# Optimization experiments

Measured on AMD Instinct MI355X. Metric: run time of the kernel, lower is better.

The kernel has to match this reference:

```python
import jax, jax.numpy as jnp
import numpy as np

IN_SIZE = 65536
HIDDEN = 128
D_STEPS = 64   # nd_actions[0]
N_ACT = 512    # nd_actions[1]


def setup_inputs() -> dict:
    key = jax.random.key(0)
    ks = jax.random.split(key, 7)
    s = 1.0 / np.sqrt(HIDDEN)  # torch LSTMCell/Linear init scale (uniform); use scaled normal
    return {
        "x": jax.random.normal(ks[0], (IN_SIZE,), jnp.float32),
        "w_ih": jax.random.normal(ks[1], (4 * HIDDEN, IN_SIZE), jnp.float32) * s,
        "w_hh": jax.random.normal(ks[2], (4 * HIDDEN, HIDDEN), jnp.float32) * s,
        "b_ih": jax.random.normal(ks[3], (4 * HIDDEN,), jnp.float32) * s,
        "b_hh": jax.random.normal(ks[4], (4 * HIDDEN,), jnp.float32) * s,
        "w_lin": jax.random.normal(ks[5], (N_ACT, HIDDEN), jnp.float32) * s,
        "b_lin": jax.random.normal(ks[6], (N_ACT,), jnp.float32) * s,
    }


def reference(x, w_ih, w_hh, b_ih, b_hh, w_lin, b_lin):
    # x is constant across the D steps, so its gate contribution is computed once.
    ihx = w_ih @ x + b_ih + b_hh  # (4H,)
    h0 = jnp.zeros((HIDDEN,), x.dtype)
    c0 = jnp.zeros((HIDDEN,), x.dtype)

    def step(carry, _):
        h, c = carry
        gates = ihx + w_hh @ h  # (4H,)
        i, f, g, o = jnp.split(gates, 4)  # torch LSTMCell gate order: i, f, g, o
        c = jax.nn.sigmoid(f) * c + jax.nn.sigmoid(i) * jnp.tanh(g)
        h = jax.nn.sigmoid(o) * jnp.tanh(c)
        logits = w_lin @ h + b_lin  # (N,)
        return (h, c), logits

    _, action_probs = jax.lax.scan(step, (h0, c0), None, length=D_STEPS)
    return action_probs  # (D, N)
```

## Files before the change

kernel.cpp:

```cpp
#include <hip/hip_runtime.h>
#include <hip/hip_bf16.h>

#define IN_SIZE 65536
#define HIDDEN 128
#define D_STEPS 64
#define N_ACT 512

typedef _Float16 half2_ __attribute__((ext_vector_type(2)));

__device__ __forceinline__ float dot2f(half2_ a, half2_ b, float c) {
#if __has_builtin(__builtin_amdgcn_fdot2)
    return __builtin_amdgcn_fdot2(a, b, c, false);
#else
    return c + (float)a[0] * (float)b[0] + (float)a[1] * (float)b[1];
#endif
}

__global__ __launch_bounds__(256) void k_ihx(const float* __restrict__ w_ih,
                                             const float* __restrict__ x,
                                             float* __restrict__ partials) {
    int bid = blockIdx.x;
    int r = bid >> 2;
    int c = bid & 3;
    int t = threadIdx.x;
    const float4* wp = (const float4*)(w_ih + (size_t)r * IN_SIZE + c * 16384);
    const float4* xp = (const float4*)(x + c * 16384);
    float acc = 0.f;
#pragma unroll
    for (int i = 0; i < 16; ++i) {
        float4 w4 = wp[t + i * 256];
        float4 x4 = xp[t + i * 256];
        acc += w4.x * x4.x + w4.y * x4.y + w4.z * x4.z + w4.w * x4.w;
    }
#pragma unroll
    for (int off = 32; off; off >>= 1) acc += __shfl_down(acc, off, 64);
    __shared__ float s[4];
    if ((t & 63) == 0) s[t >> 6] = acc;
    __syncthreads();
    if (t == 0) partials[r * 4 + c] = s[0] + s[1] + s[2] + s[3];
}

__global__ __launch_bounds__(512) void k_rec(const float* __restrict__ w_hh,
                                             const float* __restrict__ b_ih,
                                             const float* __restrict__ b_hh,
                                             const float* __restrict__ partials,
                                             float* __restrict__ h_hist) {
    int t = threadIdx.x;
    int l = t & 63;
    int gate = t & 3;
    int cell = t >> 2;
    int row = gate * HIDDEN + cell;

    half2_ wr[HIDDEN / 2];
    const float2* wp = (const float2*)(w_hh + (size_t)row * HIDDEN);
#pragma unroll
    for (int i = 0; i < HIDDEN / 2; ++i) {
        float2 v = wp[i];
        half2_ w2 = {(_Float16)v.x, (_Float16)v.y};
        wr[i] = w2;
    }
    float ihx = partials[row * 4 + 0] + partials[row * 4 + 1] +
                partials[row * 4 + 2] + partials[row * 4 + 3] +
                b_ih[row] + b_hh[row];

    __shared__ half2_ h_s[2][HIDDEN / 2];
    float c = 0.f;
    if (t < HIDDEN / 2) { half2_ z = {(_Float16)0.f, (_Float16)0.f}; h_s[0][t] = z; }
    __syncthreads();

    for (int d = 0; d < D_STEPS; ++d) {
        int rb = d & 1, wb = rb ^ 1;
        const half2_* hb = h_s[rb];
        float a0 = 0.f, a1 = 0.f, a2 = 0.f, a3 = 0.f;
#pragma unroll
        for (int i = 0; i < HIDDEN / 2; i += 4) {
            a0 = dot2f(wr[i + 0], hb[i + 0], a0);
            a1 = dot2f(wr[i + 1], hb[i + 1], a1);
            a2 = dot2f(wr[i + 2], hb[i + 2], a2);
            a3 = dot2f(wr[i + 3], hb[i + 3], a3);
        }
        float g = ihx + ((a0 + a1) + (a2 + a3));
        float kmul = (gate == 2) ? 2.f : 1.f;
        float s = 1.f / (1.f + __expf(-kmul * g));
        float act = (gate == 2) ? (2.f * s - 1.f) : s;
        int base = l & ~3;
        float ai = __shfl(act, base + 0, 64);
        float af = __shfl(act, base + 1, 64);
        float at = __shfl(act, base + 2, 64);
        float ao = __shfl(act, base + 3, 64);
        c = af * c + ai * at;
        float h = ao * (2.f / (1.f + __expf(-2.f * c)) - 1.f);
        float hp = __shfl(h, (l + 4) & 63, 64);
        if ((t & 7) == 0) { half2_ p = {(_Float16)h, (_Float16)hp}; h_s[wb][t >> 3] = p; }
        if ((t & 3) == 0) h_hist[d * HIDDEN + cell] = h;
        __syncthreads();
    }
}

__global__ __launch_bounds__(512) void k_logits(const float* __restrict__ w_lin,
                                                const float* __restrict__ b_lin,
                                                const float* __restrict__ h_hist,
                                                float* __restrict__ out) {
    int d = blockIdx.x;
    int n = threadIdx.x;
    __shared__ float h_s[HIDDEN];
    if (n < HIDDEN) h_s[n] = h_hist[d * HIDDEN + n];
    __syncthreads();
    const float4* wp = (const float4*)(w_lin + (size_t)n * HIDDEN);
    float acc = b_lin[n];
#pragma unroll
    for (int k4 = 0; k4 < HIDDEN / 4; ++k4) {
        float4 w4 = wp[k4];
        acc += w4.x * h_s[4 * k4 + 0] + w4.y * h_s[4 * k4 + 1] +
               w4.z * h_s[4 * k4 + 2] + w4.w * h_s[4 * k4 + 3];
    }
    out[d * N_ACT + n] = acc;
}

extern "C" void kernel_launch(void* const* d_in, const int* in_sizes, int n_in,
                              void* d_out, int out_size, void* d_ws, size_t ws_size,
                              hipStream_t stream) {
    const float* x     = (const float*)d_in[0];
    const float* w_ih  = (const float*)d_in[1];
    const float* w_hh  = (const float*)d_in[2];
    const float* b_ih  = (const float*)d_in[3];
    const float* b_hh  = (const float*)d_in[4];
    const float* w_lin = (const float*)d_in[5];
    const float* b_lin = (const float*)d_in[6];
    float* out = (float*)d_out;

    float* ws       = (float*)d_ws;
    float* partials = ws;
    float* h_hist   = ws + 2048;

    k_ihx<<<2048, 256, 0, stream>>>(w_ih, x, partials);
    k_rec<<<1, 512, 0, stream>>>(w_hh, b_ih, b_hh, partials, h_hist);
    k_logits<<<64, 512, 0, stream>>>(w_lin, b_lin, h_hist, out);
}
```

Before: 83.67 us.

## Fuse three kernels into one persistent kernel with global atomic barriers

Replaces the three launches (ihx GEMV, serial recurrence, logits) with one persistent 256-block kernel that uses atomic-counter grid barriers between phases. Block 0 preloads w_hh while the ihx phase runs, and the h vector moves to half8 shared storage for wider loads. The aim is to remove launch gaps and the partials round-trip. In exchange it needs a memset per call, relies on all 256 blocks being co-resident for the spin barrier, and runs the w_ih stream with fewer, larger blocks.

```diff
diff --git a/kernel.cpp b/kernel.cpp
--- a/kernel.cpp
+++ b/kernel.cpp
@@ -5,8 +5,10 @@
 #define HIDDEN 128
 #define D_STEPS 64
 #define N_ACT 512
+#define NBLK 256
 
 typedef _Float16 half2_ __attribute__((ext_vector_type(2)));
+typedef _Float16 half8_ __attribute__((ext_vector_type(8)));
 
 __device__ __forceinline__ float dot2f(half2_ a, half2_ b, float c) {
 #if __has_builtin(__builtin_amdgcn_fdot2)
@@ -16,105 +18,131 @@
 #endif
 }
 
-__global__ __launch_bounds__(256) void k_ihx(const float* __restrict__ w_ih,
-                                             const float* __restrict__ x,
-                                             float* __restrict__ partials) {
-    int bid = blockIdx.x;
-    int r = bid >> 2;
-    int c = bid & 3;
-    int t = threadIdx.x;
-    const float4* wp = (const float4*)(w_ih + (size_t)r * IN_SIZE + c * 16384);
-    const float4* xp = (const float4*)(x + c * 16384);
-    float acc = 0.f;
-#pragma unroll
-    for (int i = 0; i < 16; ++i) {
-        float4 w4 = wp[t + i * 256];
-        float4 x4 = xp[t + i * 256];
-        acc += w4.x * x4.x + w4.y * x4.y + w4.z * x4.z + w4.w * x4.w;
+__device__ __forceinline__ void gbar(int* cnt) {
+    __syncthreads();
+    if (threadIdx.x == 0) {
+        __hip_atomic_fetch_add(cnt, 1, __ATOMIC_RELEASE, __HIP_MEMORY_SCOPE_AGENT);
+        while (__hip_atomic_load(cnt, __ATOMIC_ACQUIRE, __HIP_MEMORY_SCOPE_AGENT) < NBLK)
+            __builtin_amdgcn_s_sleep(8);
     }
-#pragma unroll
-    for (int off = 32; off; off >>= 1) acc += __shfl_down(acc, off, 64);
-    __shared__ float s[4];
-    if ((t & 63) == 0) s[t >> 6] = acc;
     __syncthreads();
-    if (t == 0) partials[r * 4 + c] = s[0] + s[1] + s[2] + s[3];
 }
 
-__global__ __launch_bounds__(512) void k_rec(const float* __restrict__ w_hh,
-                                             const float* __restrict__ b_ih,
-                                             const float* __restrict__ b_hh,
-                                             const float* __restrict__ partials,
-                                             float* __restrict__ h_hist) {
+__global__ __launch_bounds__(1024, 4) void fused(
+    const float* __restrict__ x,
+    const float* __restrict__ w_ih,
+    const float* __restrict__ w_hh,
+    const float* __restrict__ b_ih,
+    const float* __restrict__ b_hh,
+    const float* __restrict__ w_lin,
+    const float* __restrict__ b_lin,
+    int* __restrict__ cnt,
+    float* __restrict__ ihx_ws,
+    float* __restrict__ h_hist,
+    float* __restrict__ out) {
     int t = threadIdx.x;
-    int l = t & 63;
-    int gate = t & 3;
-    int cell = t >> 2;
-    int row = gate * HIDDEN + cell;
+    int b = blockIdx.x;
 
     half2_ wr[HIDDEN / 2];
-    const float2* wp = (const float2*)(w_hh + (size_t)row * HIDDEN);
+    int gate = t & 3;
+    int cell = (t >> 2) & 127;
+    if (b == 0 && t < 512) {
+        const float2* wp2 = (const float2*)(w_hh + (size_t)(gate * HIDDEN + cell) * HIDDEN);
 #pragma unroll
-    for (int i = 0; i < HIDDEN / 2; ++i) {
-        float2 v = wp[i];
-        half2_ w2 = {(_Float16)v.x, (_Float16)v.y};
-        wr[i] = w2;
+        for (int i = 0; i < HIDDEN / 2; ++i) {
+            float2 v = wp2[i];
+            half2_ w2 = {(_Float16)v.x, (_Float16)v.y};
+            wr[i] = w2;
+        }
     }
-    float ihx = partials[row * 4 + 0] + partials[row * 4 + 1] +
-                partials[row * 4 + 2] + partials[row * 4 + 3] +
-                b_ih[row] + b_hh[row];
 
-    __shared__ half2_ h_s[2][HIDDEN / 2];
-    float c = 0.f;
-    if (t < HIDDEN / 2) { half2_ z = {(_Float16)0.f, (_Float16)0.f}; h_s[0][t] = z; }
-    __syncthreads();
+    {
+        int q = t >> 9;
+        int u = t & 511;
+        int row = 2 * b + q;
+        const float4* wp = (const float4*)(w_ih + (size_t)row * IN_SIZE);
+        const float4* xp = (const float4*)x;
+        float acc = 0.f;
+#pragma unroll 8
+        for (int i = 0; i < 32; ++i) {
+            float4 w4 = wp[u + i * 512];
+            float4 x4 = xp[u + i * 512];
+            acc += w4.x * x4.x + w4.y * x4.y + w4.z * x4.z + w4.w * x4.w;
+        }
+#pragma unroll
+        for (int off = 32; off; off >>= 1) acc += __shfl_down(acc, off, 64);
+        __shared__ float s[16];
+        if ((t & 63) == 0) s[t >> 6] = acc;
+        __syncthreads();
+        if ((t & 511) == 0) {
+            float v = 0.f;
+#pragma unroll
+            for (int i = 0; i < 8; ++i) v += s[(q << 3) + i];
+            ihx_ws[row] = v + b_ih[row] + b_hh[row];
+        }
+    }
+    gbar(&cnt[0]);
 
-    for (int d = 0; d < D_STEPS; ++d) {
-        int rb = d & 1, wb = rb ^ 1;
-        const half2_* hb = h_s[rb];
-        float a0 = 0.f, a1 = 0.f, a2 = 0.f, a3 = 0.f;
+    __shared__ half8_ h_v[2][HIDDEN / 8];
+    if (b == 0) {
+        int l = t & 63;
+        float ihx = 0.f, c = 0.f;
+        if (t < 512) ihx = ihx_ws[gate * HIDDEN + cell];
+        if (t < HIDDEN) ((_Float16*)&h_v[0][0])[t] = (_Float16)0.f;
+        __syncthreads();
+
+        for (int d = 0; d < D_STEPS; ++d) {
+            int rbuf = d & 1, wbuf = rbuf ^ 1;
+            if (t < 512) {
+                const half8_* hb = h_v[rbuf];
+                float a0 = 0.f, a1 = 0.f, a2 = 0.f, a3 = 0.f;
 #pragma unroll
-        for (int i = 0; i < HIDDEN / 2; i += 4) {
-            a0 = dot2f(wr[i + 0], hb[i + 0], a0);
-            a1 = dot2f(wr[i + 1], hb[i + 1], a1);
-            a2 = dot2f(wr[i + 2], hb[i + 2], a2);
-            a3 = dot2f(wr[i + 3], hb[i + 3], a3);
+                for (int i = 0; i < 16; ++i) {
+                    union { half8_ v8; half2_ p[4]; } u;
+                    u.v8 = hb[i];
+                    a0 = dot2f(wr[4 * i + 0], u.p[0], a0);
+                    a1 = dot2f(wr[4 * i + 1], u.p[1], a1);
+                    a2 = dot2f(wr[4 * i + 2], u.p[2], a2);
+                    a3 = dot2f(wr[4 * i + 3], u.p[3], a3);
+                }
+                float g = ihx + ((a0 + a1) + (a2 + a3));
+                float kmul = (gate == 2) ? 2.f : 1.f;
+                float sg = 1.f / (1.f + __expf(-kmul * g));
+                float act = (gate == 2) ? (2.f * sg - 1.f) : sg;
+                int base = l & ~3;
+                float ai = __shfl(act, base + 0, 64);
+                float af = __shfl(act, base + 1, 64);
+                float at = __shfl(act, base + 2, 64);
+                float ao = __shfl(act, base + 3, 64);
+                c = af * c + ai * at;
+                float h = ao * (2.f / (1.f + __expf(-2.f * c)) - 1.f);
+                if ((t & 3) == 0) {
+                    ((_Float16*)&h_v[wbuf][0])[cell] = (_Float16)h;
+                    h_hist[d * HIDDEN + cell] = h;
+                }
+            }
+            __syncthreads();
         }
-        float g = ihx + ((a0 + a1) + (a2 + a3));
-        float kmul = (gate == 2) ? 2.f : 1.f;
-        float s = 1.f / (1.f + __expf(-kmul * g));
-        float act = (gate == 2) ? (2.f * s - 1.f) : s;
-        int base = l & ~3;
-        float ai = __shfl(act, base + 0, 64);
-        float af = __shfl(act, base + 1, 64);
-        float at = __shfl(act, base + 2, 64);
-        float ao = __shfl(act, base + 3, 64);
-        c = af * c + ai * at;
-        float h = ao * (2.f / (1.f + __expf(-2.f * c)) - 1.f);
-        float hp = __shfl(h, (l + 4) & 63, 64);
-        if ((t & 7) == 0) { half2_ p = {(_Float16)h, (_Float16)hp}; h_s[wb][t >> 3] = p; }
-        if ((t & 3) == 0) h_hist[d * HIDDEN + cell] = h;
+    }
+    gbar(&cnt[16]);
+
+    if (b < 32) {
+        int s3 = t >> 9;
+        int d = 2 * b + s3;
+        int n = t & 511;
+        __shared__ float hs2[2][HIDDEN];
+        if ((t & 511) < HIDDEN) hs2[s3][t & 127] = h_hist[d * HIDDEN + (t & 127)];
         __syncthreads();
+        const float4* wp = (const float4*)(w_lin + (size_t)n * HIDDEN);
+        float acc = b_lin[n];
+#pragma unroll
+        for (int k = 0; k < HIDDEN / 4; ++k) {
+            float4 w4 = wp[k];
+            acc += w4.x * hs2[s3][4 * k + 0] + w4.y * hs2[s3][4 * k + 1] +
+                   w4.z * hs2[s3][4 * k + 2] + w4.w * hs2[s3][4 * k + 3];
+        }
+        out[d * N_ACT + n] = acc;
     }
-}
-
-__global__ __launch_bounds__(512) void k_logits(const float* __restrict__ w_lin,
-                                                const float* __restrict__ b_lin,
-                                                const float* __restrict__ h_hist,
-                                                float* __restrict__ out) {
-    int d = blockIdx.x;
-    int n = threadIdx.x;
-    __shared__ float h_s[HIDDEN];
-    if (n < HIDDEN) h_s[n] = h_hist[d * HIDDEN + n];
-    __syncthreads();
-    const float4* wp = (const float4*)(w_lin + (size_t)n * HIDDEN);
-    float acc = b_lin[n];
-#pragma unroll
-    for (int k4 = 0; k4 < HIDDEN / 4; ++k4) {
-        float4 w4 = wp[k4];
-        acc += w4.x * h_s[4 * k4 + 0] + w4.y * h_s[4 * k4 + 1] +
-               w4.z * h_s[4 * k4 + 2] + w4.w * h_s[4 * k4 + 3];
-    }
-    out[d * N_ACT + n] = acc;
 }
 
 extern "C" void kernel_launch(void* const* d_in, const int* in_sizes, int n_in,
@@ -129,11 +157,12 @@
     const float* b_lin = (const float*)d_in[6];
     float* out = (float*)d_out;
 
-    float* ws       = (float*)d_ws;
-    float* partials = ws;
-    float* h_hist   = ws + 2048;
+    hipMemsetAsync(d_ws, 0, 128, stream);
+    int*   cnt    = (int*)d_ws;
+    float* ws_f   = (float*)d_ws;
+    float* ihx_ws = ws_f + 32;
+    float* h_hist = ws_f + 32 + 512;
 
-    k_ihx<<<2048, 256, 0, stream>>>(w_ih, x, partials);
-    k_rec<<<1, 512, 0, stream>>>(w_hh, b_ih, b_hh, partials, h_hist);
-    k_logits<<<64, 512, 0, stream>>>(w_lin, b_lin, h_hist, out);
+    fused<<<NBLK, 1024, 0, stream>>>(x, w_ih, w_hh, b_ih, b_hh, w_lin, b_lin,
+                                     cnt, ihx_ws, h_hist, out);
 }
```

Result: slower. 130.3 us (+55.7%).
